# Kernel tuning notes

Measured on AMD Instinct MI355X. Metric: run time of the kernel, lower is better.

Reference implementation:

```python
import jax, jax.numpy as jnp
import numpy as np

B, N, P = 8, 4096, 1024
P4 = P // 4
EPS = 1e-5


def _ln(x, g, b):
    mu = jnp.mean(x, axis=-1, keepdims=True)
    var = jnp.var(x, axis=-1, keepdims=True)
    return (x - mu) * jax.lax.rsqrt(var + EPS) * g + b


def setup_inputs() -> dict:
    key = jax.random.key(0)
    ks = jax.random.split(key, 16)
    s = lambda fan: 1.0 / np.sqrt(fan)
    return {
        "xyz": jax.random.normal(ks[0], (B, N, 3), jnp.float32),
        "x": jax.random.normal(ks[1], (B, N, P), jnp.float32),
        "ln1_g": jnp.ones((P,), jnp.float32),
        "ln1_b": jnp.zeros((P,), jnp.float32),
        "ln2_g": jnp.ones((P,), jnp.float32),
        "ln2_b": jnp.zeros((P,), jnp.float32),
        "qk_w": jax.random.normal(ks[2], (P4, P), jnp.float32) * s(P),   # shared q/k 1x1 conv, no bias
        "v_w": jax.random.normal(ks[3], (P, P), jnp.float32) * s(P),
        "v_b": jax.random.normal(ks[4], (P,), jnp.float32) * s(P),
        "t1_w": jax.random.normal(ks[5], (P, P4), jnp.float32) * s(P4),  # trans_conv
        "t1_b": jax.random.normal(ks[6], (P,), jnp.float32) * s(P4),
        "t2_w": jax.random.normal(ks[7], (P, P4), jnp.float32) * s(P4),  # trans_conv1
        "t2_b": jax.random.normal(ks[8], (P,), jnp.float32) * s(P4),
        "m1_w": jax.random.normal(ks[9], (P, P), jnp.float32) * s(P),
        "m1_b": jax.random.normal(ks[10], (P,), jnp.float32) * s(P),
        "m2_w": jax.random.normal(ks[11], (P, P), jnp.float32) * s(P),
        "m2_b": jax.random.normal(ks[12], (P,), jnp.float32) * s(P),
    }


def reference(xyz, x, ln1_g, ln1_b, ln2_g, ln2_b, qk_w, v_w, v_b,
              t1_w, t1_b, t2_w, t2_b, m1_w, m1_b, m2_w, m2_b):
    # xyz is accepted but unused, matching the torch module. Dropout = eval identity.
    res1 = x
    h = _ln(x, ln1_g, ln1_b)                                   # [B,N,P]
    # TransformerBlock_1 (1x1 convs on h^T [B,P,N] are just matmuls over P)
    x_q = jnp.einsum('op,bnp->bon', qk_w, h)                   # [B,P4,N]
    # k shares weights with q; x_k permuted is x_q transposed
    x_v = jnp.einsum('op,bnp->bno', v_w, h) + v_b              # [B,N,P]
    energy = jnp.einsum('bqn,bkn->bqk', x_q, x_q)              # [B,P4,P4]
    att = jnp.einsum('op,bpk->bok', t1_w, energy) + t1_b[:, None]   # [B,P,P4]
    att = jax.nn.gelu(att, approximate=False)
    att = jnp.einsum('op,bkp->bok', t2_w, att) + t2_b[:, None]      # [B,P,P]
    att = jax.nn.softmax(att, axis=-1)
    t_out = jnp.einsum('bnp,bpq->bnq', x_v, att)               # [B,N,P]
    x1 = t_out + res1
    h2 = _ln(x1, ln2_g, ln2_b)
    m = jax.nn.gelu(h2 @ m1_w.T + m1_b, approximate=False)
    m = m @ m2_w.T + m2_b
    return x1 + m
```

## Files before the change

### kernel.cpp

```cpp
#include <hip/hip_runtime.h>


typedef __attribute__((ext_vector_type(4))) float f32x4;
typedef __attribute__((ext_vector_type(8))) _Float16 h16x8;
typedef __attribute__((ext_vector_type(8))) unsigned short u16x8;
typedef __attribute__((ext_vector_type(4))) unsigned short u16x4;

__device__ __forceinline__ unsigned short f2h(float f) {
  _Float16 h = (_Float16)f;
  return __builtin_bit_cast(unsigned short, h);
}
__device__ __forceinline__ float h2f(unsigned short u) {
  return (float)__builtin_bit_cast(_Float16, u);
}
__device__ __forceinline__ unsigned split16(float f) {
  _Float16 h = (_Float16)f;
  _Float16 l = (_Float16)(f - (float)h);
  return (unsigned)__builtin_bit_cast(unsigned short, h) |
         ((unsigned)__builtin_bit_cast(unsigned short, l) << 16);
}
__device__ __forceinline__ float gelu_f(float x) {
  return 0.5f * x * (1.0f + erff(x * 0.70710678118654752f));
}
__device__ __forceinline__ void gload16(const void* g, void* l) {
  __builtin_amdgcn_global_load_lds(
      (const __attribute__((address_space(1))) unsigned int*)g,
      (__attribute__((address_space(3))) unsigned int*)l, 16, 0, 0);
}
#define FENCE() asm volatile("" ::: "memory")

__device__ __forceinline__ void xcd_swz(int& bx, int& by, int gx, int gy) {
  const int nwg = gx * gy;
  if ((nwg & 7) == 0 && nwg >= 16) {
    const int hw = bx + gx * by;
    const int chunk = nwg >> 3;
    const int tf = (hw & 7) * chunk + (hw >> 3);
    by = tf % gy;
    bx = tf / gy;
  }
}

__global__ __launch_bounds__(256)
void ln_kernel(const float* __restrict__ x, const float* __restrict__ g,
               const float* __restrict__ b, unsigned short* __restrict__ hi,
               unsigned short* __restrict__ lo, unsigned short* __restrict__ xh) {
  __shared__ float red[16];
  const size_t base = (size_t)blockIdx.x * 1024;
  const int t = threadIdx.x;
  f32x4 v = *(const f32x4*)&x[base + t * 4];
  float s = v[0] + v[1] + v[2] + v[3];
  float q = v[0] * v[0] + v[1] * v[1] + v[2] * v[2] + v[3] * v[3];
#pragma unroll
  for (int o = 32; o > 0; o >>= 1) { s += __shfl_down(s, o); q += __shfl_down(q, o); }
  const int w = t >> 6;
  if ((t & 63) == 0) { red[w] = s; red[8 + w] = q; }
  __syncthreads();
  s = (red[0] + red[1]) + (red[2] + red[3]);
  q = (red[8] + red[9]) + (red[10] + red[11]);
  const float mu = s * (1.0f / 1024.0f);
  const float var = q * (1.0f / 1024.0f) - mu * mu;
  const float is = rsqrtf(var + 1e-5f);
  f32x4 gg = *(const f32x4*)&g[t * 4];
  f32x4 bb = *(const f32x4*)&b[t * 4];
  u16x4 oh, ol, ox;
#pragma unroll
  for (int j = 0; j < 4; j++) {
    float y = (v[j] - mu) * is * gg[j] + bb[j];
    unsigned p = split16(y);
    oh[j] = (unsigned short)(p & 0xffffu);
    ol[j] = (unsigned short)(p >> 16);
    ox[j] = f2h(v[j]);
  }
  *(u16x4*)&hi[base + t * 4] = oh;
  if (lo) *(u16x4*)&lo[base + t * 4] = ol;
  if (xh) *(u16x4*)&xh[base + t * 4] = ox;
}

__global__ __launch_bounds__(256)
void ln16_kernel(const unsigned short* __restrict__ x16, const float* __restrict__ g,
                 const float* __restrict__ b, unsigned short* __restrict__ hi) {
  __shared__ float red[16];
  const size_t base = (size_t)blockIdx.x * 1024;
  const int t = threadIdx.x;
  u16x4 raw = *(const u16x4*)&x16[base + t * 4];
  float v[4];
#pragma unroll
  for (int j = 0; j < 4; j++) v[j] = h2f(raw[j]);
  float s = v[0] + v[1] + v[2] + v[3];
  float q = v[0] * v[0] + v[1] * v[1] + v[2] * v[2] + v[3] * v[3];
#pragma unroll
  for (int o = 32; o > 0; o >>= 1) { s += __shfl_down(s, o); q += __shfl_down(q, o); }
  const int w = t >> 6;
  if ((t & 63) == 0) { red[w] = s; red[8 + w] = q; }
  __syncthreads();
  s = (red[0] + red[1]) + (red[2] + red[3]);
  q = (red[8] + red[9]) + (red[10] + red[11]);
  const float mu = s * (1.0f / 1024.0f);
  const float var = q * (1.0f / 1024.0f) - mu * mu;
  const float is = rsqrtf(var + 1e-5f);
  f32x4 gg = *(const f32x4*)&g[t * 4];
  f32x4 bb = *(const f32x4*)&b[t * 4];
  u16x4 oh;
#pragma unroll
  for (int j = 0; j < 4; j++) oh[j] = f2h((v[j] - mu) * is * gg[j] + bb[j]);
  *(u16x4*)&hi[base + t * 4] = oh;
}

__global__ __launch_bounds__(256)
void cvt_kernel(const float* __restrict__ in, unsigned short* __restrict__ hi,
                unsigned short* __restrict__ lo, int n4) {
  int i = blockIdx.x * 256 + threadIdx.x;
  if (i < n4) {
    f32x4 v = *(const f32x4*)&in[(size_t)i * 4];
    u16x4 oh, ol;
#pragma unroll
    for (int j = 0; j < 4; j++) {
      unsigned p = split16(v[j]);
      oh[j] = (unsigned short)(p & 0xffffu);
      ol[j] = (unsigned short)(p >> 16);
    }
    *(u16x4*)&hi[(size_t)i * 4] = oh;
    if (lo) *(u16x4*)&lo[(size_t)i * 4] = ol;
  }
}

__global__ __launch_bounds__(256)
void vwt_kernel(const float* __restrict__ vw, unsigned short* __restrict__ wvt) {
  __shared__ float T[64][65];
  const int bx = blockIdx.x, by = blockIdx.y;
  const int t = threadIdx.x;
  const int lr = t >> 6, lc = t & 63;
#pragma unroll
  for (int i = 0; i < 16; ++i) {
    const int row = i * 4 + lr;
    T[row][lc] = vw[(size_t)(by * 64 + row) * 1024 + bx * 64 + lc];
  }
  __syncthreads();
#pragma unroll
  for (int i = 0; i < 16; ++i) {
    const int row = i * 4 + lr;
    wvt[(size_t)(bx * 64 + row) * 1024 + by * 64 + lc] = f2h(T[lc][row]);
  }
}

__global__ __launch_bounds__(256)
void beff_kernel(const unsigned short* __restrict__ attT, const float* __restrict__ vb,
                 float* __restrict__ beff) {
  const int b = blockIdx.y;
  const int q = blockIdx.x * 4 + (threadIdx.x >> 6);
  const int l = threadIdx.x & 63;
  const unsigned short* row = attT + ((size_t)b * 1024 + q) * 1024;
  float s = 0.0f;
#pragma unroll
  for (int i = 0; i < 2; ++i) {
    u16x8 v = *(const u16x8*)&row[(i * 64 + l) * 8];
    f32x4 vb0 = *(const f32x4*)&vb[(i * 64 + l) * 8];
    f32x4 vb1 = *(const f32x4*)&vb[(i * 64 + l) * 8 + 4];
#pragma unroll
    for (int j = 0; j < 4; j++) s += h2f(v[j]) * vb0[j];
#pragma unroll
    for (int j = 0; j < 4; j++) s += h2f(v[j + 4]) * vb1[j];
  }
#pragma unroll
  for (int o = 32; o > 0; o >>= 1) s += __shfl_down(s, o);
  if (l == 0) beff[b * 1024 + q] = s;
}

template <int EPI>
__global__ __launch_bounds__(256)
void gemm_v(const unsigned short* __restrict__ Ain, const unsigned short* __restrict__ Bin,
            void* __restrict__ Cout, const float* __restrict__ bias,
            const unsigned short* __restrict__ res16In,
            int K, int lda, int ldb, int ldc,
            long long sA, long long sB, long long sC, long long sBias, long long sRes) {
  __shared__ short As[2][4096];
  __shared__ short Bs[2][4096];
  const int z = blockIdx.z;
  const unsigned short* A = Ain + (size_t)z * sA;
  const unsigned short* B = Bin + (size_t)z * sB;
  int bx = blockIdx.x, by = blockIdx.y;
  xcd_swz(bx, by, gridDim.x, gridDim.y);
  const int mBase = by * 128, nBase = bx * 128;
  const int t = threadIdx.x, w = t >> 6, l = t & 63;
  const int r16 = l & 15, kq = l >> 4;
  const int wr = (w >> 1) * 64, wc = (w & 1) * 64;
  f32x4 acc[4][4] = {};

  auto stage = [&](int buf, int k0) {
#pragma unroll
    for (int i = 0; i < 2; ++i) {
      const int c = i * 256 + t;
      const int row = c >> 2, cc = c & 3;
      const int gc = cc ^ ((row >> 1) & 3);
      short* la = &As[buf][(i * 256 + w * 64) * 8];
      short* lb = &Bs[buf][(i * 256 + w * 64) * 8];
      gload16(&A[(size_t)(mBase + row) * lda + k0 + gc * 8], la);
      gload16(&B[(size_t)(nBase + row) * ldb + k0 + gc * 8], lb);
    }
  };

  const int nt = K >> 5;
  stage(0, 0);
  if (nt > 1) stage(1, 32);
  for (int ts = 0; ts < nt; ++ts) {
    const int cur = ts & 1;
    if (ts + 1 < nt) { asm volatile("s_waitcnt vmcnt(4)" ::: "memory"); }
    else             { asm volatile("s_waitcnt vmcnt(0)" ::: "memory"); }
    __builtin_amdgcn_s_barrier();
    FENCE();
    h16x8 aF[4], bF[4];
#pragma unroll
    for (int mi = 0; mi < 4; mi++) {
      const int r = wr + mi * 16 + r16;
      aF[mi] = *(const h16x8*)&As[cur][r * 32 + (kq ^ ((r >> 1) & 3)) * 8];
    }
#pragma unroll
    for (int ni = 0; ni < 4; ni++) {
      const int r = wc + ni * 16 + r16;
      bF[ni] = *(const h16x8*)&Bs[cur][r * 32 + (kq ^ ((r >> 1) & 3)) * 8];
    }
    __builtin_amdgcn_s_setprio(1);
#pragma unroll
    for (int mi = 0; mi < 4; mi++)
#pragma unroll
      for (int ni = 0; ni < 4; ni++)
        acc[mi][ni] = __builtin_amdgcn_mfma_f32_16x16x32_f16(aF[mi], bF[ni], acc[mi][ni], 0, 0, 0);
    __builtin_amdgcn_s_setprio(0);
    FENCE();
    __builtin_amdgcn_s_barrier();
    FENCE();
    if (ts + 2 < nt) stage(cur, (ts + 2) * 32);
  }

  unsigned short* C16 = (unsigned short*)Cout + (size_t)z * sC;
  float* C32 = (float*)Cout + (size_t)z * sC;
  const float* bp = (EPI == 1 || EPI == 3 || EPI == 8) ? bias + (size_t)z * sBias : nullptr;
  const unsigned short* rp = (EPI == 3 || EPI == 8) ? res16In + (size_t)z * sRes : nullptr;
#pragma unroll
  for (int mi = 0; mi < 4; mi++) {
#pragma unroll
    for (int ni = 0; ni < 4; ni++) {
      const int cl = nBase + wc + ni * 16 + r16;
      const float bcol = bp ? bp[cl] : 0.0f;
#pragma unroll
      for (int r = 0; r < 4; r++) {
        const int rw = mBase + wr + mi * 16 + kq * 4 + r;
        float v = acc[mi][ni][r] + bcol;
        if (EPI == 1) v = gelu_f(v);
        const size_t idx = (size_t)rw * ldc + cl;
        if (EPI == 3)      C32[idx] = v + h2f(rp[idx]);
        else if (EPI == 8) C16[idx] = f2h(v + h2f(rp[idx]));
        else               C16[idx] = f2h(v);
      }
    }
  }
}

template <int EPI>
__global__ __launch_bounds__(256)
void gemm_s(const unsigned short* __restrict__ Ahi, const unsigned short* __restrict__ Alo,
            const unsigned short* __restrict__ Bhi, const unsigned short* __restrict__ Blo,
            void* __restrict__ Cout, unsigned short* __restrict__ Cout2,
            const float* __restrict__ bias,
            int K, int lda, int ldb, int ldc,
            long long sA, long long sB, long long sC, int splitK) {
  __shared__ short As[2][8192];
  __shared__ short Bs[2][8192];
  const int z = blockIdx.z;
  const int bi = z / splitK, sp = z % splitK;
  const int kLen = K / splitK, kStart = sp * kLen;
  const unsigned short* AH = Ahi + (size_t)bi * sA;
  const unsigned short* BH = Bhi + (size_t)bi * sB;
  const unsigned short* AL = Alo + (size_t)bi * sA;
  const unsigned short* BL = Blo + (size_t)bi * sB;
  int bx = blockIdx.x, by = blockIdx.y;
  xcd_swz(bx, by, gridDim.x, gridDim.y);
  const int mBase = by * 128, nBase = bx * 128;
  const int t = threadIdx.x, w = t >> 6, l = t & 63;
  const int r16 = l & 15, kq = l >> 4;
  const int wr = (w >> 1) * 64, wc = (w & 1) * 64;
  f32x4 acc[4][4] = {};

  auto stage = [&](int buf, int k0) {
#pragma unroll
    for (int i = 0; i < 2; ++i) {
      const int c = i * 256 + t;
      const int row = c >> 2, cc = c & 3;
      const int gc = cc ^ ((row >> 1) & 3);
      const int cbase = i * 256 + w * 64;
      const size_t ga = (size_t)(mBase + row) * lda + k0 + gc * 8;
      const size_t gb = (size_t)(nBase + row) * ldb + k0 + gc * 8;
      gload16(&AH[ga], &As[buf][cbase * 8]);
      gload16(&AL[ga], &As[buf][4096 + cbase * 8]);
      gload16(&BH[gb], &Bs[buf][cbase * 8]);
      gload16(&BL[gb], &Bs[buf][4096 + cbase * 8]);
    }
  };

  const int nsteps = kLen >> 5;
  stage(0, kStart);
  if (nsteps > 1) stage(1, kStart + 32);
  for (int ts = 0; ts < nsteps; ++ts) {
    const int cur = ts & 1;
    if (ts + 1 < nsteps) { asm volatile("s_waitcnt vmcnt(8)" ::: "memory"); }
    else                 { asm volatile("s_waitcnt vmcnt(0)" ::: "memory"); }
    __builtin_amdgcn_s_barrier();
    FENCE();
    h16x8 aH[4], bH[4], aL[4], bL[4];
#pragma unroll
    for (int mi = 0; mi < 4; mi++) {
      const int r = wr + mi * 16 + r16;
      const int off = r * 32 + (kq ^ ((r >> 1) & 3)) * 8;
      aH[mi] = *(const h16x8*)&As[cur][off];
      aL[mi] = *(const h16x8*)&As[cur][4096 + off];
    }
#pragma unroll
    for (int ni = 0; ni < 4; ni++) {
      const int r = wc + ni * 16 + r16;
      const int off = r * 32 + (kq ^ ((r >> 1) & 3)) * 8;
      bH[ni] = *(const h16x8*)&Bs[cur][off];
      bL[ni] = *(const h16x8*)&Bs[cur][4096 + off];
    }
    __builtin_amdgcn_s_setprio(1);
#pragma unroll
    for (int mi = 0; mi < 4; mi++)
#pragma unroll
      for (int ni = 0; ni < 4; ni++) {
        acc[mi][ni] = __builtin_amdgcn_mfma_f32_16x16x32_f16(aH[mi], bH[ni], acc[mi][ni], 0, 0, 0);
        acc[mi][ni] = __builtin_amdgcn_mfma_f32_16x16x32_f16(aH[mi], bL[ni], acc[mi][ni], 0, 0, 0);
        acc[mi][ni] = __builtin_amdgcn_mfma_f32_16x16x32_f16(aL[mi], bH[ni], acc[mi][ni], 0, 0, 0);
      }
    __builtin_amdgcn_s_setprio(0);
    FENCE();
    __builtin_amdgcn_s_barrier();
    FENCE();
    if (ts + 2 < nsteps) stage(cur, kStart + (ts + 2) * 32);
  }

  unsigned short* C16 = (unsigned short*)Cout + (size_t)z * sC;
  unsigned short* C16b = Cout2 ? Cout2 + (size_t)z * sC : nullptr;
  float* C32 = (float*)Cout + (size_t)z * sC;
#pragma unroll
  for (int mi = 0; mi < 4; mi++) {
#pragma unroll
    for (int ni = 0; ni < 4; ni++) {
      const int cl = nBase + wc + ni * 16 + r16;
#pragma unroll
      for (int r = 0; r < 4; r++) {
        const int rw = mBase + wr + mi * 16 + kq * 4 + r;
        float v = acc[mi][ni][r];
        if (EPI == 6 || EPI == 7) v += bias[rw];
        if (EPI == 6) v = gelu_f(v);
        const size_t idx = (size_t)rw * ldc + cl;
        if (EPI == 4 || EPI == 6) {
          unsigned p = split16(v);
          C16[idx] = (unsigned short)(p & 0xffffu);
          C16b[idx] = (unsigned short)(p >> 16);
        } else {
          C32[idx] = v;
        }
      }
    }
  }
}

__global__ __launch_bounds__(256)
void ereduce_kernel(const float* __restrict__ part, unsigned short* __restrict__ ehi,
                    unsigned short* __restrict__ elo) {
  const size_t idx = (size_t)blockIdx.x * 256 + threadIdx.x;
  const size_t b = idx >> 16, i = idx & 65535;
  const float* p = part + b * (8ull * 65536) + i;
  float s0 = (p[0] + p[65536]) + (p[2 * 65536] + p[3 * 65536]);
  float s1 = (p[4 * 65536] + p[5 * 65536]) + (p[6 * 65536] + p[7 * 65536]);
  unsigned pk = split16(s0 + s1);
  ehi[idx] = (unsigned short)(pk & 0xffffu);
  elo[idx] = (unsigned short)(pk >> 16);
}

__global__ __launch_bounds__(256)
void smax_t_kernel(const float* __restrict__ a2, unsigned short* __restrict__ attT) {
  __shared__ float S[8][1028];
  __shared__ float inv[8];
  const int t = threadIdx.x;
  const int b = blockIdx.y;
  const int o0 = blockIdx.x * 8;
  const float* src = a2 + ((size_t)b * 1024 + o0) * 1024;
#pragma unroll
  for (int i = 0; i < 8; i++)
    *(f32x4*)&S[i][t * 4] = *(const f32x4*)&src[(size_t)i * 1024 + t * 4];
  __syncthreads();
  const int w = t >> 6, l = t & 63;
  for (int rr = 0; rr < 2; rr++) {
    const int r = w * 2 + rr;
    float m = -1e30f;
#pragma unroll
    for (int i = 0; i < 16; i++) m = fmaxf(m, S[r][l + i * 64]);
#pragma unroll
    for (int o = 32; o > 0; o >>= 1) m = fmaxf(m, __shfl_xor(m, o));
    float ssum = 0.0f;
#pragma unroll
    for (int i = 0; i < 16; i++) {
      float e = expf(S[r][l + i * 64] - m);
      S[r][l + i * 64] = e;
      ssum += e;
    }
#pragma unroll
    for (int o = 32; o > 0; o >>= 1) ssum += __shfl_xor(ssum, o);
    if (l == 0) inv[r] = 1.0f / ssum;
  }
  __syncthreads();
  float iv[8];
#pragma unroll
  for (int r = 0; r < 8; r++) iv[r] = inv[r];
#pragma unroll
  for (int i = 0; i < 4; i++) {
    const int k = i * 256 + t;
    u16x8 ov;
#pragma unroll
    for (int r = 0; r < 8; r++) ov[r] = f2h(S[r][k] * iv[r]);
    *(u16x8*)&attT[((size_t)b * 1024 + k) * 1024 + o0] = ov;
  }
}

extern "C" void kernel_launch(void* const* d_in, const int* in_sizes, int n_in,
                              void* d_out, int out_size, void* d_ws, size_t ws_size,
                              hipStream_t stream) {
  (void)in_sizes; (void)n_in; (void)out_size; (void)ws_size;
  const float* x     = (const float*)d_in[1];
  const float* ln1_g = (const float*)d_in[2];
  const float* ln1_b = (const float*)d_in[3];
  const float* ln2_g = (const float*)d_in[4];
  const float* ln2_b = (const float*)d_in[5];
  const float* qk_w  = (const float*)d_in[6];
  const float* v_w   = (const float*)d_in[7];
  const float* v_b   = (const float*)d_in[8];
  const float* t1_w  = (const float*)d_in[9];
  const float* t1_b  = (const float*)d_in[10];
  const float* t2_w  = (const float*)d_in[11];
  const float* t2_b  = (const float*)d_in[12];
  const float* m1_w  = (const float*)d_in[13];
  const float* m1_b  = (const float*)d_in[14];
  const float* m2_w  = (const float*)d_in[15];
  const float* m2_b  = (const float*)d_in[16];

  char* ws = (char*)d_ws;
  unsigned short* hhi  = (unsigned short*)(ws + 0);
  unsigned short* hlo  = (unsigned short*)(ws + 67108864);
  unsigned short* Qthi = (unsigned short*)(ws + 134217728);
  unsigned short* Qtlo = (unsigned short*)(ws + 150994944);
  float*          part = (float*)(ws + 167772160);
  unsigned short* Ehi  = (unsigned short*)(ws + 184549376);
  unsigned short* Elo  = (unsigned short*)(ws + 185597952);
  unsigned short* Ghi  = (unsigned short*)(ws + 186646528);
  unsigned short* Glo  = (unsigned short*)(ws + 190840832);
  float*          a2   = (float*)(ws + 195035136);
  unsigned short* attT = (unsigned short*)(ws + 228589568);
  unsigned short* WeT  = (unsigned short*)(ws + 245366784);
  float*          beff = (float*)(ws + 262144000);
  unsigned short* xh   = (unsigned short*)(ws + 268435456);
  unsigned short* x1h  = (unsigned short*)(ws + 335544320);
  unsigned short* wqh  = (unsigned short*)(ws + 446693376);
  unsigned short* wql  = (unsigned short*)(ws + 447217664);
  unsigned short* wvt  = (unsigned short*)(ws + 447741952);
  unsigned short* wt1h = (unsigned short*)(ws + 449839104);
  unsigned short* wt1l = (unsigned short*)(ws + 450363392);
  unsigned short* wt2h = (unsigned short*)(ws + 450887680);
  unsigned short* wt2l = (unsigned short*)(ws + 451411968);
  unsigned short* wm1  = (unsigned short*)(ws + 451936256);
  unsigned short* wm2  = (unsigned short*)(ws + 454033408);
  unsigned short* h2 = hhi;
  unsigned short* gb = hlo;
  float* out = (float*)d_out;

  cvt_kernel<<<dim3(256),  dim3(256), 0, stream>>>(qk_w, wqh, wql, 65536);
  vwt_kernel<<<dim3(16, 16), dim3(256), 0, stream>>>(v_w, wvt);
  cvt_kernel<<<dim3(256),  dim3(256), 0, stream>>>(t1_w, wt1h, wt1l, 65536);
  cvt_kernel<<<dim3(256),  dim3(256), 0, stream>>>(t2_w, wt2h, wt2l, 65536);
  cvt_kernel<<<dim3(1024), dim3(256), 0, stream>>>(m1_w, wm1, nullptr, 262144);
  cvt_kernel<<<dim3(1024), dim3(256), 0, stream>>>(m2_w, wm2, nullptr, 262144);
  ln_kernel<<<dim3(32768), dim3(256), 0, stream>>>(x, ln1_g, ln1_b, hhi, hlo, xh);
  gemm_s<4><<<dim3(32, 2, 8), dim3(256), 0, stream>>>(
      wqh, wql, hhi, hlo, Qthi, Qtlo, nullptr,
      1024, 1024, 1024, 4096, 0, 4194304, 1048576, 1);
  gemm_s<5><<<dim3(2, 2, 64), dim3(256), 0, stream>>>(
      Qthi, Qtlo, Qthi, Qtlo, part, nullptr, nullptr,
      4096, 4096, 4096, 256, 1048576, 1048576, 65536, 8);
  ereduce_kernel<<<dim3(2048), dim3(256), 0, stream>>>(part, Ehi, Elo);
  gemm_s<6><<<dim3(2, 8, 8), dim3(256), 0, stream>>>(
      wt1h, wt1l, Ehi, Elo, Ghi, Glo, t1_b,
      256, 256, 256, 256, 0, 65536, 262144, 1);
  gemm_s<7><<<dim3(8, 8, 8), dim3(256), 0, stream>>>(
      wt2h, wt2l, Ghi, Glo, a2, nullptr, t2_b,
      256, 256, 256, 1024, 0, 262144, 1048576, 1);
  smax_t_kernel<<<dim3(128, 8), dim3(256), 0, stream>>>(a2, attT);
  gemm_v<4><<<dim3(8, 8, 8), dim3(256), 0, stream>>>(
      attT, wvt, WeT, nullptr, nullptr,
      1024, 1024, 1024, 1024, 1048576, 0, 1048576, 0, 0);
  beff_kernel<<<dim3(256, 8), dim3(256), 0, stream>>>(attT, v_b, beff);
  gemm_v<8><<<dim3(8, 32, 8), dim3(256), 0, stream>>>(
      hhi, WeT, x1h, beff, xh,
      1024, 1024, 1024, 1024, 4194304, 1048576, 4194304, 1024, 4194304);
  ln16_kernel<<<dim3(32768), dim3(256), 0, stream>>>(x1h, ln2_g, ln2_b, h2);
  gemm_v<1><<<dim3(8, 256, 1), dim3(256), 0, stream>>>(
      h2, wm1, gb, m1_b, nullptr, 1024, 1024, 1024, 1024, 0, 0, 0, 0, 0);
  gemm_v<3><<<dim3(8, 256, 1), dim3(256), 0, stream>>>(
      gb, wm2, out, m2_b, x1h, 1024, 1024, 1024, 1024, 0, 0, 0, 0, 0);
}
```

Measured before the change: 684.0 us.

## Stage GEMM epilogues through LDS for vectorized 16-byte fp16 stores

The fp16-output GEMM epilogues now write each wave's 64x64 accumulator tile into its own LDS region, then read it back row-contiguously and issue 16-byte global stores, with the residual add done on 8-wide vectors. This replaces the scattered 2-byte per-element stores of the MFMA output layout. The split-hi/lo epilogue does the same twice, once for each half. The XCD block swizzle also changes its remapping to decompose along gx instead of gy, which changes which tiles share an XCD and its L2. The LDS reuse relies on the last loop barrier and no cross-wave reads, since each wave touches only its own region.

```diff
diff --git a/kernel.cpp b/kernel.cpp
--- a/kernel.cpp
+++ b/kernel.cpp
@@ -32,11 +32,11 @@
 __device__ __forceinline__ void xcd_swz(int& bx, int& by, int gx, int gy) {
   const int nwg = gx * gy;
   if ((nwg & 7) == 0 && nwg >= 16) {
-    const int hw = bx + gx * by;
+    const int flat = bx + gx * by;
     const int chunk = nwg >> 3;
-    const int tf = (hw & 7) * chunk + (hw >> 3);
-    by = tf % gy;
-    bx = tf / gy;
+    const int nf = (flat & 7) * chunk + (flat >> 3);
+    bx = nf % gx;
+    by = nf / gx;
   }
 }
 
@@ -231,26 +231,55 @@
     FENCE();
     if (ts + 2 < nt) stage(cur, (ts + 2) * 32);
   }
+  FENCE();
 
   unsigned short* C16 = (unsigned short*)Cout + (size_t)z * sC;
   float* C32 = (float*)Cout + (size_t)z * sC;
   const float* bp = (EPI == 1 || EPI == 3 || EPI == 8) ? bias + (size_t)z * sBias : nullptr;
   const unsigned short* rp = (EPI == 3 || EPI == 8) ? res16In + (size_t)z * sRes : nullptr;
-#pragma unroll
-  for (int mi = 0; mi < 4; mi++) {
-#pragma unroll
-    for (int ni = 0; ni < 4; ni++) {
-      const int cl = nBase + wc + ni * 16 + r16;
-      const float bcol = bp ? bp[cl] : 0.0f;
-#pragma unroll
-      for (int r = 0; r < 4; r++) {
-        const int rw = mBase + wr + mi * 16 + kq * 4 + r;
-        float v = acc[mi][ni][r] + bcol;
-        if (EPI == 1) v = gelu_f(v);
-        const size_t idx = (size_t)rw * ldc + cl;
-        if (EPI == 3)      C32[idx] = v + h2f(rp[idx]);
-        else if (EPI == 8) C16[idx] = f2h(v + h2f(rp[idx]));
-        else               C16[idx] = f2h(v);
+
+  if constexpr (EPI == 1 || EPI == 4 || EPI == 8) {
+    short* ep = ((w & 2) ? &Bs[0][0] : &As[0][0]) + (w & 1) * 4096;
+#pragma unroll
+    for (int mi = 0; mi < 4; mi++) {
+#pragma unroll
+      for (int ni = 0; ni < 4; ni++) {
+        const int cl = nBase + wc + ni * 16 + r16;
+        const float bcol = bp ? bp[cl] : 0.0f;
+#pragma unroll
+        for (int r = 0; r < 4; r++) {
+          float v = acc[mi][ni][r] + bcol;
+          if (EPI == 1) v = gelu_f(v);
+          ep[(mi * 16 + kq * 4 + r) * 64 + ni * 16 + r16] = (short)f2h(v);
+        }
+      }
+    }
+#pragma unroll
+    for (int j = 0; j < 8; j++) {
+      const int f = j * 512 + l * 8;
+      const int row = f >> 6, col = f & 63;
+      u16x8 v8 = *(const u16x8*)&ep[f];
+      const size_t gi = (size_t)(mBase + wr + row) * ldc + nBase + wc + col;
+      if (EPI == 8) {
+        u16x8 r8 = *(const u16x8*)&rp[gi];
+#pragma unroll
+        for (int q = 0; q < 8; q++) v8[q] = f2h(h2f(v8[q]) + h2f(r8[q]));
+      }
+      *(u16x8*)&C16[gi] = v8;
+    }
+  } else {
+#pragma unroll
+    for (int mi = 0; mi < 4; mi++) {
+#pragma unroll
+      for (int ni = 0; ni < 4; ni++) {
+        const int cl = nBase + wc + ni * 16 + r16;
+        const float bcol = bp[cl];
+#pragma unroll
+        for (int r = 0; r < 4; r++) {
+          const int rw = mBase + wr + mi * 16 + kq * 4 + r;
+          const size_t idx = (size_t)rw * ldc + cl;
+          C32[idx] = acc[mi][ni][r] + bcol + h2f(rp[idx]);
+        }
       }
     }
   }
@@ -336,28 +365,67 @@
     FENCE();
     if (ts + 2 < nsteps) stage(cur, kStart + (ts + 2) * 32);
   }
+  FENCE();
 
   unsigned short* C16 = (unsigned short*)Cout + (size_t)z * sC;
   unsigned short* C16b = Cout2 ? Cout2 + (size_t)z * sC : nullptr;
   float* C32 = (float*)Cout + (size_t)z * sC;
-#pragma unroll
-  for (int mi = 0; mi < 4; mi++) {
-#pragma unroll
-    for (int ni = 0; ni < 4; ni++) {
-      const int cl = nBase + wc + ni * 16 + r16;
-#pragma unroll
-      for (int r = 0; r < 4; r++) {
-        const int rw = mBase + wr + mi * 16 + kq * 4 + r;
-        float v = acc[mi][ni][r];
-        if (EPI == 6 || EPI == 7) v += bias[rw];
-        if (EPI == 6) v = gelu_f(v);
-        const size_t idx = (size_t)rw * ldc + cl;
-        if (EPI == 4 || EPI == 6) {
-          unsigned p = split16(v);
-          C16[idx] = (unsigned short)(p & 0xffffu);
-          C16b[idx] = (unsigned short)(p >> 16);
-        } else {
-          C32[idx] = v;
+
+  if constexpr (EPI == 4 || EPI == 6) {
+    short* ep = &As[0][0] + w * 4096;
+    unsigned pk[4][4][4];
+#pragma unroll
+    for (int mi = 0; mi < 4; mi++)
+#pragma unroll
+      for (int ni = 0; ni < 4; ni++)
+#pragma unroll
+        for (int r = 0; r < 4; r++) {
+          float v = acc[mi][ni][r];
+          if (EPI == 6) { v += bias[mBase + wr + mi * 16 + kq * 4 + r]; v = gelu_f(v); }
+          pk[mi][ni][r] = split16(v);
+        }
+#pragma unroll
+    for (int mi = 0; mi < 4; mi++)
+#pragma unroll
+      for (int ni = 0; ni < 4; ni++)
+#pragma unroll
+        for (int r = 0; r < 4; r++)
+          ep[(mi * 16 + kq * 4 + r) * 64 + ni * 16 + r16] =
+              (short)(pk[mi][ni][r] & 0xffffu);
+#pragma unroll
+    for (int j = 0; j < 8; j++) {
+      const int f = j * 512 + l * 8;
+      const int row = f >> 6, col = f & 63;
+      *(u16x8*)&C16[(size_t)(mBase + wr + row) * ldc + nBase + wc + col] =
+          *(const u16x8*)&ep[f];
+    }
+#pragma unroll
+    for (int mi = 0; mi < 4; mi++)
+#pragma unroll
+      for (int ni = 0; ni < 4; ni++)
+#pragma unroll
+        for (int r = 0; r < 4; r++)
+          ep[(mi * 16 + kq * 4 + r) * 64 + ni * 16 + r16] =
+              (short)(pk[mi][ni][r] >> 16);
+#pragma unroll
+    for (int j = 0; j < 8; j++) {
+      const int f = j * 512 + l * 8;
+      const int row = f >> 6, col = f & 63;
+      *(u16x8*)&C16b[(size_t)(mBase + wr + row) * ldc + nBase + wc + col] =
+          *(const u16x8*)&ep[f];
+    }
+  } else {
+#pragma unroll
+    for (int mi = 0; mi < 4; mi++) {
+#pragma unroll
+      for (int ni = 0; ni < 4; ni++) {
+        const int cl = nBase + wc + ni * 16 + r16;
+#pragma unroll
+        for (int r = 0; r < 4; r++) {
+          const int rw = mBase + wr + mi * 16 + kq * 4 + r;
+          float v = acc[mi][ni][r];
+          if (EPI == 7) v += bias[rw];
+          C32[(size_t)rw * ldc + cl] = v;
         }
       }
     }
```

Result: faster. 655.0 us (-4.2%).
